# Performance work log

Hardware: AMD Instinct MI355X
Metric: run time of the kernel (lower is better)

## Reference

```python
import jax, jax.numpy as jnp
import numpy as np

MU = 1.0          # stability parameter
DT = 0.01         # Euler step
EPS = 1e-9        # matches E in the torch source
BOUND = float(np.pi / 2)  # hard_bounds = (-pi/2, pi/2)
N_NODES = 200_000
N_EDGES = 12_800_000  # avg degree 64


def setup_inputs() -> dict:
    key = jax.random.key(0)
    ks = jax.random.split(key, 9)
    n, ne = N_NODES, N_EDGES
    # distributions mirror the torch initialization
    x = jax.random.normal(ks[0], (n,), jnp.float32) * 0.1
    y = jax.random.normal(ks[1], (n,), jnp.float32) * 0.1
    w = (jax.random.uniform(ks[2], (n,), jnp.float32) * 2 - 1) * 4.0 + 2.0
    amplitudes = (jax.random.uniform(ks[3], (n,), jnp.float32) * 2 - 1) * 2.0 + 1.0
    phase = (jax.random.uniform(ks[4], (n,), jnp.float32) * 2 - 1) * np.pi
    ha = jax.random.normal(ks[5], (n,), jnp.float32) * 0.5
    b = jax.random.normal(ks[6], (n,), jnp.float32) * 0.1
    edge_src = jax.random.randint(ks[7], (ne,), 0, n, jnp.int32)
    edge_dst = jax.random.randint(ks[8], (ne,), 0, n, jnp.int32)
    return {"x": x, "y": y, "w": w, "amplitudes": amplitudes, "phase": phase,
            "ha": ha, "b": b, "edge_src": edge_src, "edge_dst": edge_dst}


def reference(x, y, w, amplitudes, phase, ha, b, edge_src, edge_dst):
    n = x.shape[0]
    # r^2 = x^2 + y^2 + E  (torch computes sqrt(..+E) then squares it)
    r2 = x * x + y * y + EPS
    dx = (MU - r2) * x - w * y
    dy = (MU - r2) * y + w * x
    # edge coupling: for edge (j=src -> i=dst):
    #   d*_i += ha_i * sin(theta_j - theta_i) * (*_j - *_i)
    theta = jnp.arctan2(y, x + EPS)                       # [n]
    coef = ha[edge_dst] * jnp.sin(theta[edge_src] - theta[edge_dst])  # [ne]
    cx = jax.ops.segment_sum(coef * (x[edge_src] - x[edge_dst]), edge_dst, num_segments=n)
    cy = jax.ops.segment_sum(coef * (y[edge_src] - y[edge_dst]), edge_dst, num_segments=n)
    # Euler step (x update is internal state; angles depend only on new y)
    y_new = y + (dy + cy) * DT
    x_new = x + (dx + cx) * DT
    angles = amplitudes * y_new + phase + b
    angles = jnp.clip(angles, -BOUND, BOUND)
    return angles
```

## Files before the change

kernel.cpp:

```cpp
#include <hip/hip_runtime.h>
#include <hip/hip_bf16.h>

#define MU_V    1.0f
#define DT_V    0.01f
#define EPS_V   1e-9f
#define BOUND_V 1.5707963267948966f

constexpr int NPB     = 2048;
constexpr int LOG_NPB = 11;
constexpr int NB_MAX  = 128;
constexpr int B1      = 512;
constexpr int EPT     = 16;
constexpr int EPB     = B1 * EPT;
constexpr int CAP     = 136192;
constexpr int RB      = 256;

__global__ void node_pre_kernel(const float* __restrict__ x_,
                                const float* __restrict__ y_,
                                const float* __restrict__ ha_,
                                float4* __restrict__ pack,
                                unsigned* __restrict__ zbuf,
                                int n, int nz) {
    int i = blockIdx.x * blockDim.x + threadIdx.x;
    if (i < nz) zbuf[i] = 0u;
    if (i >= n) return;
    float x = x_[i];
    float y = y_[i];
    float xe = x + EPS_V;
    float r2 = xe * xe + y * y;
    float s, c;
    if (r2 > 0.0f) {
        float rinv = rsqrtf(r2);
        s = y * rinv;
        c = xe * rinv;
    } else {
        s = 0.0f;
        c = 1.0f;
    }
    pack[i] = make_float4(s, c, y, ha_[i]);
}

__global__ __launch_bounds__(B1)
void bucket_scatter_kernel(const int* __restrict__ src,
                           const int* __restrict__ dst,
                           unsigned* __restrict__ cursors,
                           unsigned* __restrict__ buf,
                           int ne, int nb) {
    __shared__ unsigned cnt[NB_MAX];
    __shared__ unsigned gbase[NB_MAX];
    __shared__ unsigned loc[NB_MAX];
    int tid = threadIdx.x;
    for (int i = tid; i < nb; i += B1) cnt[i] = 0u;
    __syncthreads();
    long long base = (long long)blockIdx.x * EPB;
    #pragma unroll
    for (int it = 0; it < EPT / 4; ++it) {
        long long e = base + ((long long)(it * B1 + tid)) * 4;
        if (e + 4 <= ne) {
            int4 d4 = *(const int4*)(dst + e);
            atomicAdd(&cnt[((unsigned)d4.x) >> LOG_NPB], 1u);
            atomicAdd(&cnt[((unsigned)d4.y) >> LOG_NPB], 1u);
            atomicAdd(&cnt[((unsigned)d4.z) >> LOG_NPB], 1u);
            atomicAdd(&cnt[((unsigned)d4.w) >> LOG_NPB], 1u);
        } else if (e < ne) {
            for (long long q = e; q < ne; ++q)
                atomicAdd(&cnt[((unsigned)dst[q]) >> LOG_NPB], 1u);
        }
    }
    __syncthreads();
    for (int b = tid; b < nb; b += B1) {
        unsigned c = cnt[b];
        gbase[b] = c ? atomicAdd(&cursors[b], c) : 0u;
        loc[b] = 0u;
    }
    __syncthreads();
    #pragma unroll
    for (int it = 0; it < EPT / 4; ++it) {
        long long e = base + ((long long)(it * B1 + tid)) * 4;
        if (e + 4 <= ne) {
            int4 s4 = *(const int4*)(src + e);
            int4 d4 = *(const int4*)(dst + e);
            {
                unsigned d = (unsigned)d4.x, s = (unsigned)s4.x, b = d >> LOG_NPB;
                unsigned pos = gbase[b] + atomicAdd(&loc[b], 1u);
                if (pos < (unsigned)CAP) buf[(size_t)b * CAP + pos] = (s << LOG_NPB) | (d & (NPB - 1));
            }
            {
                unsigned d = (unsigned)d4.y, s = (unsigned)s4.y, b = d >> LOG_NPB;
                unsigned pos = gbase[b] + atomicAdd(&loc[b], 1u);
                if (pos < (unsigned)CAP) buf[(size_t)b * CAP + pos] = (s << LOG_NPB) | (d & (NPB - 1));
            }
            {
                unsigned d = (unsigned)d4.z, s = (unsigned)s4.z, b = d >> LOG_NPB;
                unsigned pos = gbase[b] + atomicAdd(&loc[b], 1u);
                if (pos < (unsigned)CAP) buf[(size_t)b * CAP + pos] = (s << LOG_NPB) | (d & (NPB - 1));
            }
            {
                unsigned d = (unsigned)d4.w, s = (unsigned)s4.w, b = d >> LOG_NPB;
                unsigned pos = gbase[b] + atomicAdd(&loc[b], 1u);
                if (pos < (unsigned)CAP) buf[(size_t)b * CAP + pos] = (s << LOG_NPB) | (d & (NPB - 1));
            }
        } else if (e < ne) {
            for (long long q = e; q < ne; ++q) {
                unsigned d = (unsigned)dst[q], s = (unsigned)src[q], b = d >> LOG_NPB;
                unsigned pos = gbase[b] + atomicAdd(&loc[b], 1u);
                if (pos < (unsigned)CAP) buf[(size_t)b * CAP + pos] = (s << LOG_NPB) | (d & (NPB - 1));
            }
        }
    }
}

__device__ __forceinline__ void reduce_entry(unsigned ent,
                                             const float4* __restrict__ pack,
                                             const float4* __restrict__ plocal,
                                             float* __restrict__ acc) {
    unsigned s  = ent >> LOG_NPB;
    unsigned dl = ent & (NPB - 1);
    float4 ps = pack[s];
    float4 pd = plocal[dl];
    float v = (pd.w * (ps.x * pd.y - ps.y * pd.x)) * (ps.z - pd.z);
    atomicAdd(&acc[dl], v);
}

__global__ __launch_bounds__(RB)
void bucket_reduce_kernel(const unsigned* __restrict__ cursors,
                          const unsigned* __restrict__ buf,
                          const float4* __restrict__ pack,
                          float* __restrict__ partial, int n, int nsub) {
    __shared__ float4 plocal[NPB];
    __shared__ float  acc[NPB];
    int b   = blockIdx.x / nsub;
    int sub = blockIdx.x % nsub;
    int tid = threadIdx.x;
    int node0 = b << LOG_NPB;
    for (int k = tid; k < NPB; k += RB) {
        int d = node0 + k;
        plocal[k] = (d < n) ? pack[d] : make_float4(0.f, 0.f, 0.f, 0.f);
        acc[k] = 0.0f;
    }
    __syncthreads();
    unsigned count = cursors[b];
    if (count > (unsigned)CAP) count = (unsigned)CAP;
    unsigned chunk = (((count + nsub - 1) / nsub) + 7u) & ~7u;
    unsigned lo = (unsigned)sub * chunk;
    unsigned hi = lo + chunk;
    if (hi > count) hi = count;
    unsigned span = (hi > lo) ? (hi - lo) : 0u;
    unsigned vend = lo + (span & ~7u);
    const unsigned* mybuf = buf + (size_t)b * CAP;
    for (unsigned i = lo + (unsigned)tid * 8u; i < vend; i += (unsigned)RB * 8u) {
        uint4 a4 = *(const uint4*)(mybuf + i);
        uint4 b4 = *(const uint4*)(mybuf + i + 4);
        reduce_entry(a4.x, pack, plocal, acc);
        reduce_entry(a4.y, pack, plocal, acc);
        reduce_entry(a4.z, pack, plocal, acc);
        reduce_entry(a4.w, pack, plocal, acc);
        reduce_entry(b4.x, pack, plocal, acc);
        reduce_entry(b4.y, pack, plocal, acc);
        reduce_entry(b4.z, pack, plocal, acc);
        reduce_entry(b4.w, pack, plocal, acc);
    }
    {
        unsigned idx = vend + (unsigned)tid;
        if (idx < hi)
            reduce_entry(mybuf[idx], pack, plocal, acc);
    }
    __syncthreads();
    float* myp = partial + ((size_t)b * nsub + sub) * NPB;
    for (int k = tid; k < NPB; k += RB) myp[k] = acc[k];
}

__device__ __forceinline__ void edge_one(int s, int d,
                                         const float4* __restrict__ pack,
                                         float* __restrict__ cy) {
    float4 ps = pack[s];
    float4 pd = pack[d];
    float v = (pd.w * (ps.x * pd.y - ps.y * pd.x)) * (ps.z - pd.z);
    atomicAdd(&cy[d], v);
}

__global__ void edge_kernel(const int* __restrict__ src,
                            const int* __restrict__ dst,
                            const float4* __restrict__ pack,
                            float* __restrict__ cy, int ne) {
    int t = blockIdx.x * blockDim.x + threadIdx.x;
    long long base = (long long)t * 4;
    if (base >= ne) return;
    if (base + 4 <= ne) {
        int4 s4 = *(const int4*)(src + base);
        int4 d4 = *(const int4*)(dst + base);
        edge_one(s4.x, d4.x, pack, cy);
        edge_one(s4.y, d4.y, pack, cy);
        edge_one(s4.z, d4.z, pack, cy);
        edge_one(s4.w, d4.w, pack, cy);
    } else {
        for (long long e = base; e < ne; ++e)
            edge_one(src[e], dst[e], pack, cy);
    }
}

__global__ void finalize_fast_kernel(const float* __restrict__ x_,
                                     const float* __restrict__ y_,
                                     const float* __restrict__ w_,
                                     const float* __restrict__ amp_,
                                     const float* __restrict__ ph_,
                                     const float* __restrict__ b_,
                                     const float* __restrict__ partial,
                                     float* __restrict__ out, int n, int nsub) {
    int i = blockIdx.x * blockDim.x + threadIdx.x;
    if (i >= n) return;
    int bk = i >> LOG_NPB;
    int dl = i & (NPB - 1);
    float cy = 0.0f;
    for (int s = 0; s < nsub; ++s)
        cy += partial[((size_t)bk * nsub + s) * NPB + dl];
    float x = x_[i];
    float y = y_[i];
    float w = w_[i];
    float r2 = x * x + y * y + EPS_V;
    float dy = (MU_V - r2) * y + w * x;
    float y_new = y + (dy + cy) * DT_V;
    float ang = amp_[i] * y_new + ph_[i] + b_[i];
    ang = fminf(fmaxf(ang, -BOUND_V), BOUND_V);
    out[i] = ang;
}

__global__ void finalize_kernel(const float* __restrict__ x_,
                                const float* __restrict__ y_,
                                const float* __restrict__ w_,
                                const float* __restrict__ amp_,
                                const float* __restrict__ ph_,
                                const float* __restrict__ b_,
                                const float* __restrict__ cy,
                                float* __restrict__ out, int n) {
    int i = blockIdx.x * blockDim.x + threadIdx.x;
    if (i >= n) return;
    float x = x_[i];
    float y = y_[i];
    float w = w_[i];
    float r2 = x * x + y * y + EPS_V;
    float dy = (MU_V - r2) * y + w * x;
    float y_new = y + (dy + cy[i]) * DT_V;
    float ang = amp_[i] * y_new + ph_[i] + b_[i];
    ang = fminf(fmaxf(ang, -BOUND_V), BOUND_V);
    out[i] = ang;
}

extern "C" void kernel_launch(void* const* d_in, const int* in_sizes, int n_in,
                              void* d_out, int out_size, void* d_ws, size_t ws_size,
                              hipStream_t stream) {
    const float* x_   = (const float*)d_in[0];
    const float* y_   = (const float*)d_in[1];
    const float* w_   = (const float*)d_in[2];
    const float* amp_ = (const float*)d_in[3];
    const float* ph_  = (const float*)d_in[4];
    const float* ha_  = (const float*)d_in[5];
    const float* b_   = (const float*)d_in[6];
    const int* edge_src = (const int*)d_in[7];
    const int* edge_dst = (const int*)d_in[8];
    float* out = (float*)d_out;

    int n  = in_sizes[0];
    int ne = in_sizes[7];
    int nb = (n + NPB - 1) >> LOG_NPB;

    auto align256 = [](size_t v) { return (v + 255) & ~(size_t)255; };
    size_t off_pack    = 0;
    size_t off_cursors = align256(off_pack + (size_t)n * 16);
    size_t off_partial = align256(off_cursors + (size_t)nb * 4);

    int nsub = 0;
    size_t off_buf = 0;
    for (int cand : {16, 8, 4, 2, 1}) {
        size_t ob = align256(off_partial + (size_t)nb * cand * NPB * 4);
        if (ob + (size_t)nb * CAP * 4 <= ws_size) { nsub = cand; off_buf = ob; break; }
    }

    float4*   pack    = (float4*)((char*)d_ws + off_pack);
    unsigned* cursors = (unsigned*)((char*)d_ws + off_cursors);
    float*    cy      = (float*)((char*)d_ws + off_cursors);
    float*    partial = (float*)((char*)d_ws + off_partial);
    unsigned* buf     = (unsigned*)((char*)d_ws + off_buf);

    bool fast = (nsub > 0) && (nb <= NB_MAX) &&
                ((long long)n <= (1LL << (31 - LOG_NPB)));

    const int B = 256;
    if (fast) {
        node_pre_kernel<<<(n + B - 1) / B, B, 0, stream>>>(
            x_, y_, ha_, pack, cursors, n, nb);
        int blocks1 = (ne + EPB - 1) / EPB;
        bucket_scatter_kernel<<<blocks1, B1, 0, stream>>>(
            edge_src, edge_dst, cursors, buf, ne, nb);
        bucket_reduce_kernel<<<nb * nsub, RB, 0, stream>>>(
            cursors, buf, pack, partial, n, nsub);
        finalize_fast_kernel<<<(n + B - 1) / B, B, 0, stream>>>(
            x_, y_, w_, amp_, ph_, b_, partial, out, n, nsub);
    } else {
        node_pre_kernel<<<(n + B - 1) / B, B, 0, stream>>>(
            x_, y_, ha_, pack, (unsigned*)cy, n, n);
        int ngroups = (ne + 3) / 4;
        edge_kernel<<<(ngroups + B - 1) / B, B, 0, stream>>>(
            edge_src, edge_dst, pack, cy, ne);
        finalize_kernel<<<(n + B - 1) / B, B, 0, stream>>>(
            x_, y_, w_, amp_, ph_, b_, cy, out, n);
    }
}
```

Before: 320.5 us.

## Halve bucket size and keep edges in registers during bucket scatter

Bucket size drops from 2048 to 1024 nodes, which doubles the number of buckets and halves the per-bucket capacity. The per-bucket node window in the reduce stage is therefore smaller, and more blocks can work on it. Full blocks in the scatter kernel now load src and dst into registers once, reusing them for both the counting and the writing passes instead of reading dst twice from global memory. The atomic position claims are batched eight at a time before the stores. A subdivision count of 12 is added as a workspace fallback option. The costs are more buckets with less coherent writes and higher register pressure.

```diff
diff --git a/kernel.cpp b/kernel.cpp
--- a/kernel.cpp
+++ b/kernel.cpp
@@ -6,13 +6,13 @@
 #define EPS_V   1e-9f
 #define BOUND_V 1.5707963267948966f
 
-constexpr int NPB     = 2048;
-constexpr int LOG_NPB = 11;
-constexpr int NB_MAX  = 128;
+constexpr int NPB     = 1024;
+constexpr int LOG_NPB = 10;
+constexpr int NB_MAX  = 256;
 constexpr int B1      = 512;
 constexpr int EPT     = 16;
 constexpr int EPB     = B1 * EPT;
-constexpr int CAP     = 136192;
+constexpr int CAP     = 68608;
 constexpr int RB      = 256;
 
 __global__ void node_pre_kernel(const float* __restrict__ x_,
@@ -53,58 +53,98 @@
     for (int i = tid; i < nb; i += B1) cnt[i] = 0u;
     __syncthreads();
     long long base = (long long)blockIdx.x * EPB;
-    #pragma unroll
-    for (int it = 0; it < EPT / 4; ++it) {
-        long long e = base + ((long long)(it * B1 + tid)) * 4;
-        if (e + 4 <= ne) {
-            int4 d4 = *(const int4*)(dst + e);
-            atomicAdd(&cnt[((unsigned)d4.x) >> LOG_NPB], 1u);
-            atomicAdd(&cnt[((unsigned)d4.y) >> LOG_NPB], 1u);
-            atomicAdd(&cnt[((unsigned)d4.z) >> LOG_NPB], 1u);
-            atomicAdd(&cnt[((unsigned)d4.w) >> LOG_NPB], 1u);
-        } else if (e < ne) {
-            for (long long q = e; q < ne; ++q)
-                atomicAdd(&cnt[((unsigned)dst[q]) >> LOG_NPB], 1u);
-        }
-    }
-    __syncthreads();
-    for (int b = tid; b < nb; b += B1) {
-        unsigned c = cnt[b];
-        gbase[b] = c ? atomicAdd(&cursors[b], c) : 0u;
-        loc[b] = 0u;
-    }
-    __syncthreads();
-    #pragma unroll
-    for (int it = 0; it < EPT / 4; ++it) {
-        long long e = base + ((long long)(it * B1 + tid)) * 4;
-        if (e + 4 <= ne) {
-            int4 s4 = *(const int4*)(src + e);
-            int4 d4 = *(const int4*)(dst + e);
-            {
-                unsigned d = (unsigned)d4.x, s = (unsigned)s4.x, b = d >> LOG_NPB;
-                unsigned pos = gbase[b] + atomicAdd(&loc[b], 1u);
-                if (pos < (unsigned)CAP) buf[(size_t)b * CAP + pos] = (s << LOG_NPB) | (d & (NPB - 1));
+
+    if (base + EPB <= ne) {
+        int4 rs4[EPT / 4], rd4[EPT / 4];
+        #pragma unroll
+        for (int it = 0; it < EPT / 4; ++it) {
+            long long e = base + ((long long)(it * B1 + tid)) * 4;
+            rs4[it] = *(const int4*)(src + e);
+            rd4[it] = *(const int4*)(dst + e);
+        }
+        const int* sv = (const int*)rs4;
+        const int* dv = (const int*)rd4;
+        #pragma unroll
+        for (int k = 0; k < EPT; ++k)
+            atomicAdd(&cnt[((unsigned)dv[k]) >> LOG_NPB], 1u);
+        __syncthreads();
+        for (int b = tid; b < nb; b += B1) {
+            unsigned c = cnt[b];
+            gbase[b] = c ? atomicAdd(&cursors[b], c) : 0u;
+            loc[b] = 0u;
+        }
+        __syncthreads();
+        #pragma unroll
+        for (int g = 0; g < EPT / 8; ++g) {
+            unsigned pos[8], bb[8];
+            #pragma unroll
+            for (int j = 0; j < 8; ++j) {
+                unsigned d = (unsigned)dv[g * 8 + j];
+                bb[j] = d >> LOG_NPB;
+                pos[j] = gbase[bb[j]] + atomicAdd(&loc[bb[j]], 1u);
             }
-            {
-                unsigned d = (unsigned)d4.y, s = (unsigned)s4.y, b = d >> LOG_NPB;
-                unsigned pos = gbase[b] + atomicAdd(&loc[b], 1u);
-                if (pos < (unsigned)CAP) buf[(size_t)b * CAP + pos] = (s << LOG_NPB) | (d & (NPB - 1));
+            #pragma unroll
+            for (int j = 0; j < 8; ++j) {
+                unsigned d = (unsigned)dv[g * 8 + j];
+                unsigned s = (unsigned)sv[g * 8 + j];
+                if (pos[j] < (unsigned)CAP)
+                    buf[(size_t)bb[j] * CAP + pos[j]] = (s << LOG_NPB) | (d & (NPB - 1));
             }
-            {
-                unsigned d = (unsigned)d4.z, s = (unsigned)s4.z, b = d >> LOG_NPB;
-                unsigned pos = gbase[b] + atomicAdd(&loc[b], 1u);
-                if (pos < (unsigned)CAP) buf[(size_t)b * CAP + pos] = (s << LOG_NPB) | (d & (NPB - 1));
+        }
+    } else {
+        #pragma unroll
+        for (int it = 0; it < EPT / 4; ++it) {
+            long long e = base + ((long long)(it * B1 + tid)) * 4;
+            if (e + 4 <= ne) {
+                int4 d4 = *(const int4*)(dst + e);
+                atomicAdd(&cnt[((unsigned)d4.x) >> LOG_NPB], 1u);
+                atomicAdd(&cnt[((unsigned)d4.y) >> LOG_NPB], 1u);
+                atomicAdd(&cnt[((unsigned)d4.z) >> LOG_NPB], 1u);
+                atomicAdd(&cnt[((unsigned)d4.w) >> LOG_NPB], 1u);
+            } else if (e < ne) {
+                for (long long q = e; q < ne; ++q)
+                    atomicAdd(&cnt[((unsigned)dst[q]) >> LOG_NPB], 1u);
             }
-            {
-                unsigned d = (unsigned)d4.w, s = (unsigned)s4.w, b = d >> LOG_NPB;
-                unsigned pos = gbase[b] + atomicAdd(&loc[b], 1u);
-                if (pos < (unsigned)CAP) buf[(size_t)b * CAP + pos] = (s << LOG_NPB) | (d & (NPB - 1));
-            }
-        } else if (e < ne) {
-            for (long long q = e; q < ne; ++q) {
-                unsigned d = (unsigned)dst[q], s = (unsigned)src[q], b = d >> LOG_NPB;
-                unsigned pos = gbase[b] + atomicAdd(&loc[b], 1u);
-                if (pos < (unsigned)CAP) buf[(size_t)b * CAP + pos] = (s << LOG_NPB) | (d & (NPB - 1));
+        }
+        __syncthreads();
+        for (int b = tid; b < nb; b += B1) {
+            unsigned c = cnt[b];
+            gbase[b] = c ? atomicAdd(&cursors[b], c) : 0u;
+            loc[b] = 0u;
+        }
+        __syncthreads();
+        #pragma unroll
+        for (int it = 0; it < EPT / 4; ++it) {
+            long long e = base + ((long long)(it * B1 + tid)) * 4;
+            if (e + 4 <= ne) {
+                int4 s4 = *(const int4*)(src + e);
+                int4 d4 = *(const int4*)(dst + e);
+                {
+                    unsigned d = (unsigned)d4.x, s = (unsigned)s4.x, b = d >> LOG_NPB;
+                    unsigned pos = gbase[b] + atomicAdd(&loc[b], 1u);
+                    if (pos < (unsigned)CAP) buf[(size_t)b * CAP + pos] = (s << LOG_NPB) | (d & (NPB - 1));
+                }
+                {
+                    unsigned d = (unsigned)d4.y, s = (unsigned)s4.y, b = d >> LOG_NPB;
+                    unsigned pos = gbase[b] + atomicAdd(&loc[b], 1u);
+                    if (pos < (unsigned)CAP) buf[(size_t)b * CAP + pos] = (s << LOG_NPB) | (d & (NPB - 1));
+                }
+                {
+                    unsigned d = (unsigned)d4.z, s = (unsigned)s4.z, b = d >> LOG_NPB;
+                    unsigned pos = gbase[b] + atomicAdd(&loc[b], 1u);
+                    if (pos < (unsigned)CAP) buf[(size_t)b * CAP + pos] = (s << LOG_NPB) | (d & (NPB - 1));
+                }
+                {
+                    unsigned d = (unsigned)d4.w, s = (unsigned)s4.w, b = d >> LOG_NPB;
+                    unsigned pos = gbase[b] + atomicAdd(&loc[b], 1u);
+                    if (pos < (unsigned)CAP) buf[(size_t)b * CAP + pos] = (s << LOG_NPB) | (d & (NPB - 1));
+                }
+            } else if (e < ne) {
+                for (long long q = e; q < ne; ++q) {
+                    unsigned d = (unsigned)dst[q], s = (unsigned)src[q], b = d >> LOG_NPB;
+                    unsigned pos = gbase[b] + atomicAdd(&loc[b], 1u);
+                    if (pos < (unsigned)CAP) buf[(size_t)b * CAP + pos] = (s << LOG_NPB) | (d & (NPB - 1));
+                }
             }
         }
     }
@@ -271,7 +311,7 @@
 
     int nsub = 0;
     size_t off_buf = 0;
-    for (int cand : {16, 8, 4, 2, 1}) {
+    for (int cand : {16, 12, 8, 4, 2, 1}) {
         size_t ob = align256(off_partial + (size_t)nb * cand * NPB * 4);
         if (ob + (size_t)nb * CAP * 4 <= ws_size) { nsub = cand; off_buf = ob; break; }
     }
```

After: 283.1 us. -11.7%, faster.
